# Kernel tuning notes

Hardware: AMD Instinct MI355X
Metric: run time of the kernel (lower is better)

The kernel has to match this reference:

```python
import jax, jax.numpy as jnp
import numpy as np

N_NODES = 50000
IN_CH = 32
OUT_SHAPE = (2, 2)
N_EDGES = 1_600_000


def setup_inputs() -> dict:
    key = jax.random.key(0)
    k1, k2, k3 = jax.random.split(key, 3)
    x = jax.random.normal(k1, (N_NODES, IN_CH), dtype=jnp.float32)
    edge_index = jax.random.randint(k2, (2, N_EDGES), 0, N_NODES, dtype=jnp.int64)
    k = int(np.prod(OUT_SHAPE))
    # nn.Parameter initialized as identity, tiled over prod(out_shape); add small
    # noise so gradients/outputs are non-degenerate.
    tensor = (jnp.tile(jnp.eye(IN_CH, dtype=jnp.float32)[None], (k, 1, 1))
              + 0.01 * jax.random.normal(k3, (k, IN_CH, IN_CH), dtype=jnp.float32))
    return {"x": x, "edge_index": edge_index, "tensor": tensor}


def reference(x, edge_index, tensor):
    # Gather source / destination node features per edge (irregular access).
    src, dst = edge_index[0], edge_index[1]
    x_src = x[src]            # [E, C]
    x_dst = x[dst]            # [E, C]
    # Quadratic form per output entry k: maps[e, k] = x_src[e] @ T[k] @ x_dst[e]
    maps = jnp.einsum('ei,kij,ej->ek', x_src, tensor, x_dst)  # [E, K]
    return jnp.tanh(maps).reshape(-1, OUT_SHAPE[0], OUT_SHAPE[1])  # [E, 2, 2]
```

## Files before the change

kernel.cpp:

```cpp
#include <hip/hip_runtime.h>
#include <hip/hip_fp16.h>
#include <math.h>

#define IN_CH 32
#define K_OUT 4

typedef _Float16 h2_t __attribute__((ext_vector_type(2)));

__device__ __forceinline__ float dot2acc(unsigned int a, unsigned int b, float c) {
#if defined(__has_builtin)
#if __has_builtin(__builtin_amdgcn_fdot2)
    return __builtin_amdgcn_fdot2(__builtin_bit_cast(h2_t, a),
                                  __builtin_bit_cast(h2_t, b), c, false);
#else
    __half2 ha = *(__half2*)&a, hb = *(__half2*)&b;
    float2 fa = __half22float2(ha), fb = __half22float2(hb);
    return fmaf(fa.y, fb.y, fmaf(fa.x, fb.x, c));
#endif
#else
    __half2 ha = *(__half2*)&a, hb = *(__half2*)&b;
    float2 fa = __half22float2(ha), fb = __half22float2(hb);
    return fmaf(fa.y, fb.y, fmaf(fa.x, fb.x, c));
#endif
}

__global__ void prep_kernel(const float* __restrict__ x,
                            const float* __restrict__ T,
                            __half* __restrict__ z16,
                            __half* __restrict__ x16,
                            int n_nodes) {
    __shared__ float Ts[K_OUT * IN_CH * IN_CH];
    for (int t = threadIdx.x; t < K_OUT * IN_CH * IN_CH; t += blockDim.x)
        Ts[t] = T[t];
    __syncthreads();

    const int ki = threadIdx.x;
    const float* Trow = Ts + ki * IN_CH;

    for (int n = blockIdx.x; n < n_nodes; n += gridDim.x) {
        const float* xr = x + (size_t)n * IN_CH;
        float sum = 0.f;
#pragma unroll
        for (int j = 0; j < IN_CH; ++j)
            sum = fmaf(Trow[j], xr[j], sum);
        z16[(size_t)n * (K_OUT * IN_CH) + ki] = __float2half(sum);
        if (ki < IN_CH)
            x16[(size_t)n * IN_CH + ki] = __float2half(xr[ki]);
    }
}

__global__ __launch_bounds__(256)
void edge_kernel_quad16(const __half* __restrict__ x16,
                        const __half* __restrict__ z16,
                        const int* __restrict__ src,
                        const int* __restrict__ dst,
                        float* __restrict__ out,
                        int n_edges) {
    const int t = blockIdx.x * blockDim.x + threadIdx.x;
    const int e = t >> 2;
    const int l = t & 3;
    if (e >= n_edges) return;

    const int s = src[e];
    const int d = dst[e];

    const uint4 xv = ((const uint4*)x16)[(size_t)s * 4 + l];
    const uint4* zrow = (const uint4*)z16 + (size_t)d * 16;
    const uint4 z0 = zrow[0 + l];
    const uint4 z1 = zrow[4 + l];
    const uint4 z2 = zrow[8 + l];
    const uint4 z3 = zrow[12 + l];

    float p0 = 0.f, p1 = 0.f, p2 = 0.f, p3 = 0.f;
    p0 = dot2acc(xv.x, z0.x, p0); p0 = dot2acc(xv.y, z0.y, p0);
    p0 = dot2acc(xv.z, z0.z, p0); p0 = dot2acc(xv.w, z0.w, p0);

    p1 = dot2acc(xv.x, z1.x, p1); p1 = dot2acc(xv.y, z1.y, p1);
    p1 = dot2acc(xv.z, z1.z, p1); p1 = dot2acc(xv.w, z1.w, p1);

    p2 = dot2acc(xv.x, z2.x, p2); p2 = dot2acc(xv.y, z2.y, p2);
    p2 = dot2acc(xv.z, z2.z, p2); p2 = dot2acc(xv.w, z2.w, p2);

    p3 = dot2acc(xv.x, z3.x, p3); p3 = dot2acc(xv.y, z3.y, p3);
    p3 = dot2acc(xv.z, z3.z, p3); p3 = dot2acc(xv.w, z3.w, p3);

    float send01 = (l & 1) ? p0 : p1;
    float recv01 = __shfl_xor(send01, 1);
    float a01 = ((l & 1) ? p1 : p0) + recv01;
    float send23 = (l & 1) ? p2 : p3;
    float recv23 = __shfl_xor(send23, 1);
    float a23 = ((l & 1) ? p3 : p2) + recv23;
    float send = (l & 2) ? a01 : a23;
    float recv = __shfl_xor(send, 2);
    float r = ((l & 2) ? a23 : a01) + recv;

    out[t] = tanhf(r);
}

__global__ void edge_direct_kernel(const float* __restrict__ x,
                                   const float* __restrict__ T,
                                   const int* __restrict__ src,
                                   const int* __restrict__ dst,
                                   float* __restrict__ out,
                                   int n_edges) {
    int e = blockIdx.x * blockDim.x + threadIdx.x;
    if (e >= n_edges) return;

    const int s = src[e];
    const int d = dst[e];

    float xs[IN_CH], xd[IN_CH];
#pragma unroll
    for (int j = 0; j < IN_CH; ++j) {
        xs[j] = x[(size_t)s * IN_CH + j];
        xd[j] = x[(size_t)d * IN_CH + j];
    }

    float resv[K_OUT];
#pragma unroll
    for (int k = 0; k < K_OUT; ++k) {
        float acc = 0.f;
        for (int i = 0; i < IN_CH; ++i) {
            const float* Trow = T + ((size_t)k * IN_CH + i) * IN_CH;
            float yi = 0.f;
#pragma unroll
            for (int j = 0; j < IN_CH; ++j)
                yi = fmaf(Trow[j], xd[j], yi);
            acc = fmaf(xs[i], yi, acc);
        }
        resv[k] = tanhf(acc);
    }
    ((float4*)out)[e] = make_float4(resv[0], resv[1], resv[2], resv[3]);
}

extern "C" void kernel_launch(void* const* d_in, const int* in_sizes, int n_in,
                              void* d_out, int out_size, void* d_ws, size_t ws_size,
                              hipStream_t stream) {
    const float* x  = (const float*)d_in[0];
    const int*   ei = (const int*)d_in[1];
    const float* T  = (const float*)d_in[2];
    float* out      = (float*)d_out;

    const int n_nodes = in_sizes[0] / IN_CH;
    const int n_edges = in_sizes[1] / 2;
    const int* src = ei;
    const int* dst = ei + n_edges;

    const size_t z16_bytes = (size_t)n_nodes * K_OUT * IN_CH * sizeof(__half);
    const size_t x16_off   = (z16_bytes + 255) & ~(size_t)255;
    const size_t need      = x16_off + (size_t)n_nodes * IN_CH * sizeof(__half);

    const int threads = 256;

    if (ws_size >= need) {
        __half* z16 = (__half*)d_ws;
        __half* x16 = (__half*)((char*)d_ws + x16_off);

        prep_kernel<<<2048, 128, 0, stream>>>(x, T, z16, x16, n_nodes);

        const long long total = (long long)n_edges * 4;
        const int blocks = (int)((total + threads - 1) / threads);
        edge_kernel_quad16<<<blocks, threads, 0, stream>>>(
            x16, z16, src, dst, out, n_edges);
    } else {
        const int eblocks = (n_edges + threads - 1) / threads;
        edge_direct_kernel<<<eblocks, threads, 0, stream>>>(x, T, src, dst, out, n_edges);
    }
}
```

Baseline: 98.04 us.

## Restructure node prep into register-resident T waves and separate fp16 convert

The node precompute kernel is split in two: a vectorized fp32-to-fp16 conversion kernel for x, and a z kernel where each wave handles one node. In the z kernel each lane keeps two rows of T in registers and prefetches the next node's x row while computing, replacing the shared-memory T staging and the scalar per-thread dot product. The edge kernel also switches index loads and output stores to nontemporal accesses to reduce cache pollution from streaming data. This adds one extra launch and heavier register use in the prep stage.

```diff
diff --git a/kernel.cpp b/kernel.cpp
--- a/kernel.cpp
+++ b/kernel.cpp
@@ -24,28 +24,93 @@
 #endif
 }
 
-__global__ void prep_kernel(const float* __restrict__ x,
-                            const float* __restrict__ T,
-                            __half* __restrict__ z16,
-                            __half* __restrict__ x16,
-                            int n_nodes) {
-    __shared__ float Ts[K_OUT * IN_CH * IN_CH];
-    for (int t = threadIdx.x; t < K_OUT * IN_CH * IN_CH; t += blockDim.x)
-        Ts[t] = T[t];
-    __syncthreads();
-
-    const int ki = threadIdx.x;
-    const float* Trow = Ts + ki * IN_CH;
-
-    for (int n = blockIdx.x; n < n_nodes; n += gridDim.x) {
-        const float* xr = x + (size_t)n * IN_CH;
-        float sum = 0.f;
-#pragma unroll
-        for (int j = 0; j < IN_CH; ++j)
-            sum = fmaf(Trow[j], xr[j], sum);
-        z16[(size_t)n * (K_OUT * IN_CH) + ki] = __float2half(sum);
-        if (ki < IN_CH)
-            x16[(size_t)n * IN_CH + ki] = __float2half(xr[ki]);
+__global__ __launch_bounds__(256)
+void prep_z_kernel(const float* __restrict__ x,
+                   const float* __restrict__ T,
+                   __half* __restrict__ z16,
+                   int n_nodes, int total_waves) {
+    const int wid = (blockIdx.x * blockDim.x + threadIdx.x) >> 6;
+    const int l   = threadIdx.x & 63;
+
+    const float4* Ta = (const float4*)(T + (size_t)(2 * l) * IN_CH);
+    const float4* Tb = (const float4*)(T + (size_t)(2 * l + 1) * IN_CH);
+    float4 ta0 = Ta[0], ta1 = Ta[1], ta2 = Ta[2], ta3 = Ta[3];
+    float4 ta4 = Ta[4], ta5 = Ta[5], ta6 = Ta[6], ta7 = Ta[7];
+    float4 tb0 = Tb[0], tb1 = Tb[1], tb2 = Tb[2], tb3 = Tb[3];
+    float4 tb4 = Tb[4], tb5 = Tb[5], tb6 = Tb[6], tb7 = Tb[7];
+
+    int n = wid;
+    if (n >= n_nodes) return;
+
+    const float4* xr = (const float4*)(x + (size_t)n * IN_CH);
+    float4 c0 = xr[0], c1 = xr[1], c2 = xr[2], c3 = xr[3];
+    float4 c4 = xr[4], c5 = xr[5], c6 = xr[6], c7 = xr[7];
+
+    for (;;) {
+        const int nn = n + total_waves;
+        const bool has = nn < n_nodes;
+        const float4* xp = (const float4*)(x + (size_t)(has ? nn : n) * IN_CH);
+        float4 p0 = xp[0], p1 = xp[1], p2 = xp[2], p3 = xp[3];
+        float4 p4 = xp[4], p5 = xp[5], p6 = xp[6], p7 = xp[7];
+
+        float ua = 0.f, ub = 0.f, va = 0.f, vb = 0.f;
+        ua = fmaf(ta0.x, c0.x, ua); ub = fmaf(ta0.y, c0.y, ub);
+        ua = fmaf(ta0.z, c0.z, ua); ub = fmaf(ta0.w, c0.w, ub);
+        ua = fmaf(ta1.x, c1.x, ua); ub = fmaf(ta1.y, c1.y, ub);
+        ua = fmaf(ta1.z, c1.z, ua); ub = fmaf(ta1.w, c1.w, ub);
+        ua = fmaf(ta2.x, c2.x, ua); ub = fmaf(ta2.y, c2.y, ub);
+        ua = fmaf(ta2.z, c2.z, ua); ub = fmaf(ta2.w, c2.w, ub);
+        ua = fmaf(ta3.x, c3.x, ua); ub = fmaf(ta3.y, c3.y, ub);
+        ua = fmaf(ta3.z, c3.z, ua); ub = fmaf(ta3.w, c3.w, ub);
+        ua = fmaf(ta4.x, c4.x, ua); ub = fmaf(ta4.y, c4.y, ub);
+        ua = fmaf(ta4.z, c4.z, ua); ub = fmaf(ta4.w, c4.w, ub);
+        ua = fmaf(ta5.x, c5.x, ua); ub = fmaf(ta5.y, c5.y, ub);
+        ua = fmaf(ta5.z, c5.z, ua); ub = fmaf(ta5.w, c5.w, ub);
+        ua = fmaf(ta6.x, c6.x, ua); ub = fmaf(ta6.y, c6.y, ub);
+        ua = fmaf(ta6.z, c6.z, ua); ub = fmaf(ta6.w, c6.w, ub);
+        ua = fmaf(ta7.x, c7.x, ua); ub = fmaf(ta7.y, c7.y, ub);
+        ua = fmaf(ta7.z, c7.z, ua); ub = fmaf(ta7.w, c7.w, ub);
+
+        va = fmaf(tb0.x, c0.x, va); vb = fmaf(tb0.y, c0.y, vb);
+        va = fmaf(tb0.z, c0.z, va); vb = fmaf(tb0.w, c0.w, vb);
+        va = fmaf(tb1.x, c1.x, va); vb = fmaf(tb1.y, c1.y, vb);
+        va = fmaf(tb1.z, c1.z, va); vb = fmaf(tb1.w, c1.w, vb);
+        va = fmaf(tb2.x, c2.x, va); vb = fmaf(tb2.y, c2.y, vb);
+        va = fmaf(tb2.z, c2.z, va); vb = fmaf(tb2.w, c2.w, vb);
+        va = fmaf(tb3.x, c3.x, va); vb = fmaf(tb3.y, c3.y, vb);
+        va = fmaf(tb3.z, c3.z, va); vb = fmaf(tb3.w, c3.w, vb);
+        va = fmaf(tb4.x, c4.x, va); vb = fmaf(tb4.y, c4.y, vb);
+        va = fmaf(tb4.z, c4.z, va); vb = fmaf(tb4.w, c4.w, vb);
+        va = fmaf(tb5.x, c5.x, va); vb = fmaf(tb5.y, c5.y, vb);
+        va = fmaf(tb5.z, c5.z, va); vb = fmaf(tb5.w, c5.w, vb);
+        va = fmaf(tb6.x, c6.x, va); vb = fmaf(tb6.y, c6.y, vb);
+        va = fmaf(tb6.z, c6.z, va); vb = fmaf(tb6.w, c6.w, vb);
+        va = fmaf(tb7.x, c7.x, va); vb = fmaf(tb7.y, c7.y, vb);
+        va = fmaf(tb7.z, c7.z, va); vb = fmaf(tb7.w, c7.w, vb);
+
+        ((__half2*)(z16 + (size_t)n * (K_OUT * IN_CH)))[l] =
+            __floats2half2_rn(ua + ub, va + vb);
+
+        if (!has) break;
+        n = nn;
+        c0 = p0; c1 = p1; c2 = p2; c3 = p3;
+        c4 = p4; c5 = p5; c6 = p6; c7 = p7;
+    }
+}
+
+__global__ __launch_bounds__(256)
+void x16_convert_kernel(const float* __restrict__ x,
+                        __half* __restrict__ x16,
+                        int total4) {
+    for (int i = blockIdx.x * blockDim.x + threadIdx.x; i < total4;
+         i += gridDim.x * blockDim.x) {
+        float4 v = ((const float4*)x)[i];
+        __half2 h0 = __floats2half2_rn(v.x, v.y);
+        __half2 h1 = __floats2half2_rn(v.z, v.w);
+        uint2 pack;
+        pack.x = *(unsigned int*)&h0;
+        pack.y = *(unsigned int*)&h1;
+        ((uint2*)x16)[i] = pack;
     }
 }
 
@@ -61,8 +126,8 @@
     const int l = t & 3;
     if (e >= n_edges) return;
 
-    const int s = src[e];
-    const int d = dst[e];
+    const int s = __builtin_nontemporal_load(src + e);
+    const int d = __builtin_nontemporal_load(dst + e);
 
     const uint4 xv = ((const uint4*)x16)[(size_t)s * 4 + l];
     const uint4* zrow = (const uint4*)z16 + (size_t)d * 16;
@@ -94,7 +159,7 @@
     float recv = __shfl_xor(send, 2);
     float r = ((l & 2) ? a23 : a01) + recv;
 
-    out[t] = tanhf(r);
+    __builtin_nontemporal_store(tanhf(r), out + t);
 }
 
 __global__ void edge_direct_kernel(const float* __restrict__ x,
@@ -156,7 +221,12 @@
         __half* z16 = (__half*)d_ws;
         __half* x16 = (__half*)((char*)d_ws + x16_off);
 
-        prep_kernel<<<2048, 128, 0, stream>>>(x, T, z16, x16, n_nodes);
+        const int total4 = (n_nodes * IN_CH) / 4;
+        x16_convert_kernel<<<1024, threads, 0, stream>>>(x, x16, total4);
+
+        const int pblocks = 1024;
+        const int total_waves = pblocks * (threads / 64);
+        prep_z_kernel<<<pblocks, threads, 0, stream>>>(x, T, z16, n_nodes, total_waves);
 
         const long long total = (long long)n_edges * 4;
         const int blocks = (int)((total + threads - 1) / threads);
```

Measured after the change: 102.2 us. 1.04x slower.

## Restructure prep kernel with register-resident T rows and prefetched node batches

Applied to the files above, without the earlier changes.

The prep kernel now keeps four rows of T in registers per lane and processes batches of 8 nodes per wave. Each batch is staged through LDS with a software-prefetched float4 load of the next batch, and z16 and x16 are written as packed half4 stores. This replaces the old one-node-per-block loop that reread T from shared memory and loaded x with scalar accesses. The edge kernel also switches the index loads and output stores to nontemporal builtins to reduce cache pollution. The cost is high register pressure (128 floats of T per lane), which may lower occupancy.

```diff
diff --git a/kernel.cpp b/kernel.cpp
--- a/kernel.cpp
+++ b/kernel.cpp
@@ -4,6 +4,9 @@
 
 #define IN_CH 32
 #define K_OUT 4
+#define KI (K_OUT * IN_CH)
+#define BATCH_NODES 8
+#define BATCH_FLOATS (BATCH_NODES * IN_CH)
 
 typedef _Float16 h2_t __attribute__((ext_vector_type(2)));
 
@@ -24,28 +27,93 @@
 #endif
 }
 
-__global__ void prep_kernel(const float* __restrict__ x,
-                            const float* __restrict__ T,
-                            __half* __restrict__ z16,
-                            __half* __restrict__ x16,
-                            int n_nodes) {
-    __shared__ float Ts[K_OUT * IN_CH * IN_CH];
-    for (int t = threadIdx.x; t < K_OUT * IN_CH * IN_CH; t += blockDim.x)
-        Ts[t] = T[t];
-    __syncthreads();
-
-    const int ki = threadIdx.x;
-    const float* Trow = Ts + ki * IN_CH;
-
-    for (int n = blockIdx.x; n < n_nodes; n += gridDim.x) {
-        const float* xr = x + (size_t)n * IN_CH;
-        float sum = 0.f;
-#pragma unroll
-        for (int j = 0; j < IN_CH; ++j)
-            sum = fmaf(Trow[j], xr[j], sum);
-        z16[(size_t)n * (K_OUT * IN_CH) + ki] = __float2half(sum);
-        if (ki < IN_CH)
-            x16[(size_t)n * IN_CH + ki] = __float2half(xr[ki]);
+__global__ __launch_bounds__(128)
+void prep_kernel(const float* __restrict__ x,
+                 const float* __restrict__ T,
+                 __half* __restrict__ z16,
+                 __half* __restrict__ x16,
+                 int n_nodes, int total_waves) {
+    __shared__ float lds[2][BATCH_FLOATS];
+    const int wv = threadIdx.x >> 6;
+    const int l  = threadIdx.x & 63;
+    const int gwave = (blockIdx.x * (blockDim.x >> 6)) + wv;
+
+    const int kbase = (l & 31) * 4;
+    float tr[4][IN_CH];
+#pragma unroll
+    for (int r = 0; r < 4; ++r) {
+        const float4* Tp = (const float4*)(T + (size_t)(kbase + r) * IN_CH);
+#pragma unroll
+        for (int q = 0; q < 8; ++q) {
+            float4 v = Tp[q];
+            tr[r][q * 4 + 0] = v.x; tr[r][q * 4 + 1] = v.y;
+            tr[r][q * 4 + 2] = v.z; tr[r][q * 4 + 3] = v.w;
+        }
+    }
+
+    const long long ftotal = (long long)n_nodes * IN_CH;
+    const int n_batches = (n_nodes + BATCH_NODES - 1) / BATCH_NODES;
+
+    int b = gwave;
+    if (b >= n_batches) return;
+
+    long long fidx = (long long)b * BATCH_FLOATS + l * 4;
+    long long fclamp = fidx + 4 > ftotal ? ftotal - 4 : fidx;
+    float4 stg = *(const float4*)(x + fclamp);
+    bool st_ok = (fidx == fclamp);
+
+    while (true) {
+        ((float4*)lds[wv])[l] = stg;
+
+        if (st_ok) {
+            __half2 h0 = __floats2half2_rn(stg.x, stg.y);
+            __half2 h1 = __floats2half2_rn(stg.z, stg.w);
+            uint2 pk;
+            pk.x = *(unsigned int*)&h0;
+            pk.y = *(unsigned int*)&h1;
+            *(uint2*)(x16 + fidx) = pk;
+        }
+
+        const int bn = b + total_waves;
+        if (bn < n_batches) {
+            fidx = (long long)bn * BATCH_FLOATS + l * 4;
+            fclamp = fidx + 4 > ftotal ? ftotal - 4 : fidx;
+            stg = *(const float4*)(x + fclamp);
+            st_ok = (fidx == fclamp);
+        }
+
+#pragma unroll
+        for (int p = 0; p < 4; ++p) {
+            const int lrow = p * 2 + (l >> 5);
+            const int node = b * BATCH_NODES + lrow;
+            const float4* xrow = (const float4*)(lds[wv] + lrow * IN_CH);
+
+            float a0 = 0.f, a1 = 0.f, a2 = 0.f, a3 = 0.f;
+#pragma unroll
+            for (int q = 0; q < 8; ++q) {
+                float4 xq = xrow[q];
+                a0 = fmaf(tr[0][q*4+0], xq.x, a0); a0 = fmaf(tr[0][q*4+1], xq.y, a0);
+                a0 = fmaf(tr[0][q*4+2], xq.z, a0); a0 = fmaf(tr[0][q*4+3], xq.w, a0);
+                a1 = fmaf(tr[1][q*4+0], xq.x, a1); a1 = fmaf(tr[1][q*4+1], xq.y, a1);
+                a1 = fmaf(tr[1][q*4+2], xq.z, a1); a1 = fmaf(tr[1][q*4+3], xq.w, a1);
+                a2 = fmaf(tr[2][q*4+0], xq.x, a2); a2 = fmaf(tr[2][q*4+1], xq.y, a2);
+                a2 = fmaf(tr[2][q*4+2], xq.z, a2); a2 = fmaf(tr[2][q*4+3], xq.w, a2);
+                a3 = fmaf(tr[3][q*4+0], xq.x, a3); a3 = fmaf(tr[3][q*4+1], xq.y, a3);
+                a3 = fmaf(tr[3][q*4+2], xq.z, a3); a3 = fmaf(tr[3][q*4+3], xq.w, a3);
+            }
+
+            if (node < n_nodes) {
+                __half2 ha = __floats2half2_rn(a0, a1);
+                __half2 hb = __floats2half2_rn(a2, a3);
+                uint2 pk;
+                pk.x = *(unsigned int*)&ha;
+                pk.y = *(unsigned int*)&hb;
+                *(uint2*)(z16 + (size_t)node * KI + kbase) = pk;
+            }
+        }
+
+        if (bn >= n_batches) break;
+        b = bn;
     }
 }
 
@@ -61,8 +129,8 @@
     const int l = t & 3;
     if (e >= n_edges) return;
 
-    const int s = src[e];
-    const int d = dst[e];
+    const int s = __builtin_nontemporal_load(src + e);
+    const int d = __builtin_nontemporal_load(dst + e);
 
     const uint4 xv = ((const uint4*)x16)[(size_t)s * 4 + l];
     const uint4* zrow = (const uint4*)z16 + (size_t)d * 16;
@@ -94,7 +162,7 @@
     float recv = __shfl_xor(send, 2);
     float r = ((l & 2) ? a23 : a01) + recv;
 
-    out[t] = tanhf(r);
+    __builtin_nontemporal_store(tanhf(r), out + t);
 }
 
 __global__ void edge_direct_kernel(const float* __restrict__ x,
@@ -146,17 +214,19 @@
     const int* src = ei;
     const int* dst = ei + n_edges;
 
-    const size_t z16_bytes = (size_t)n_nodes * K_OUT * IN_CH * sizeof(__half);
+    const size_t z16_bytes = (size_t)n_nodes * KI * sizeof(__half);
     const size_t x16_off   = (z16_bytes + 255) & ~(size_t)255;
     const size_t need      = x16_off + (size_t)n_nodes * IN_CH * sizeof(__half);
 
     const int threads = 256;
 
-    if (ws_size >= need) {
+    if (ws_size >= need && n_nodes >= BATCH_NODES) {
         __half* z16 = (__half*)d_ws;
         __half* x16 = (__half*)((char*)d_ws + x16_off);
 
-        prep_kernel<<<2048, 128, 0, stream>>>(x, T, z16, x16, n_nodes);
+        const int pblocks = 1024;
+        const int total_waves = pblocks * 2;
+        prep_kernel<<<pblocks, 128, 0, stream>>>(x, T, z16, x16, n_nodes, total_waves);
 
         const long long total = (long long)n_edges * 4;
         const int blocks = (int)((total + threads - 1) / threads);
```

Measured after the change: 90.82 us (median of 2 runs). 1.08x faster.
